# Optimization experiments

Measured on AMD Instinct MI355X. Metric: run time of the kernel, lower is better.

The kernel has to match this reference:

```python
import jax, jax.numpy as jnp
import numpy as np

N = 50000
E = 800000
IN_C = 128
HID = 8
OUT_C = 32
HEADS = (4, 4, 4)
NEG_SLOPE = 0.2


def gat_conv(x, src, dst, W, att_src, att_dst, bias, heads, out_c, concat):
    # x: [N, F_in]; W: [F_in, heads*out_c]; att_*: [heads, out_c]; bias: [heads*out_c] or [out_c]
    n = x.shape[0]
    h = (x @ W).reshape(n, heads, out_c)                      # [N, H, C]
    a_src = (h * att_src).sum(-1)                             # [N, H]
    a_dst = (h * att_dst).sum(-1)                             # [N, H]
    e = jax.nn.leaky_relu(a_src[src] + a_dst[dst], NEG_SLOPE)  # [E, H]
    # segment softmax over edges grouped by destination node
    m = jax.ops.segment_max(e, dst, num_segments=n)           # [N, H]
    m = jnp.where(jnp.isfinite(m), m, 0.0)
    p = jnp.exp(e - m[dst])                                   # [E, H]
    s = jax.ops.segment_sum(p, dst, num_segments=n)           # [N, H]
    alpha = p / (s[dst] + 1e-16)                              # [E, H]
    msg = h[src] * alpha[:, :, None]                          # [E, H, C]
    out = jax.ops.segment_sum(msg, dst, num_segments=n)       # [N, H, C]
    out = out.reshape(n, heads * out_c) if concat else out.mean(axis=1)
    return out + bias


def setup_inputs() -> dict:
    key = jax.random.key(0)
    ks = jax.random.split(key, 16)
    x = jax.random.normal(ks[0], (N, IN_C), dtype=jnp.float32)
    edge_index = jax.random.randint(ks[1], (2, E), 0, N, dtype=jnp.int64)
    c1 = HID                       # per-head out of conv1 (8)
    c2 = HID * HEADS[0]            # per-head out of conv2 (32)
    c3 = OUT_C                     # per-head out of conv3 (32)
    in2 = HID * HEADS[0]           # 32
    in3 = HID * HEADS[0] * HEADS[1]  # 128
    sc = 0.1
    return {
        "x": x,
        "edge_index": edge_index,
        "W1": jax.random.normal(ks[2], (IN_C, HEADS[0] * c1), dtype=jnp.float32) * sc,
        "as1": jax.random.normal(ks[3], (HEADS[0], c1), dtype=jnp.float32) * sc,
        "ad1": jax.random.normal(ks[4], (HEADS[0], c1), dtype=jnp.float32) * sc,
        "b1": jnp.zeros((HEADS[0] * c1,), dtype=jnp.float32),
        "W2": jax.random.normal(ks[5], (in2, HEADS[1] * c2), dtype=jnp.float32) * sc,
        "as2": jax.random.normal(ks[6], (HEADS[1], c2), dtype=jnp.float32) * sc,
        "ad2": jax.random.normal(ks[7], (HEADS[1], c2), dtype=jnp.float32) * sc,
        "b2": jnp.zeros((HEADS[1] * c2,), dtype=jnp.float32),
        "W3": jax.random.normal(ks[8], (in3, HEADS[2] * c3), dtype=jnp.float32) * sc,
        "as3": jax.random.normal(ks[9], (HEADS[2], c3), dtype=jnp.float32) * sc,
        "ad3": jax.random.normal(ks[10], (HEADS[2], c3), dtype=jnp.float32) * sc,
        "b3": jnp.zeros((c3,), dtype=jnp.float32),
    }


def reference(x, edge_index, W1, as1, ad1, b1, W2, as2, ad2, b2, W3, as3, ad3, b3):
    src, dst = edge_index[0], edge_index[1]
    h = gat_conv(x, src, dst, W1, as1, ad1, b1, HEADS[0], HID, True)
    h = jax.nn.elu(h)
    h = gat_conv(h, src, dst, W2, as2, ad2, b2, HEADS[1], HID * HEADS[0], True)
    h = jax.nn.elu(h)
    out = gat_conv(h, src, dst, W3, as3, ad3, b3, HEADS[2], OUT_C, False)
    return out
```

## Files before the change

kernel.cpp:

```cpp
#include <hip/hip_runtime.h>
#include <hip/hip_fp16.h>

#define NEG_SLOPE 0.2f

static inline int cdiv(long long a, long long b) { return (int)((a + b - 1) / b); }

typedef _Float16 f16x8 __attribute__((ext_vector_type(8)));
typedef float f32x4 __attribute__((ext_vector_type(4)));

union h4u {
    float2  f2;
    __half2 h2[2];
};
union h8u {
    f16x8   v;
    __half2 h2[4];
};

__device__ __forceinline__ void load_sd(const void* ei_raw, int is64, int e, int E_,
                                        int& s, int& d)
{
    if (is64) {
        const long long* p = (const long long*)ei_raw;
        s = (int)p[e];
        d = (int)p[E_ + e];
    } else {
        const int* p = (const int*)ei_raw;
        s = p[e];
        d = p[E_ + e];
    }
}

__global__ __launch_bounds__(256) void prep_kernel(
    const void* __restrict__ ei, int E_, int n, int* __restrict__ flag,
    int* __restrict__ deg,
    const float* __restrict__ W1, __half* __restrict__ Wt1,
    const float* __restrict__ W2, __half* __restrict__ Wt2,
    const float* __restrict__ W3, __half* __restrict__ Wt3)
{
    int idx = blockIdx.x * 256 + threadIdx.x;

    if (blockIdx.x == 0) {
        __shared__ int bad;
        if (threadIdx.x == 0) bad = 0;
        __syncthreads();
        const long long* e64 = (const long long*)ei;
        int cnt = E_ < 512 ? E_ : 512;
        bool ok = true;
        for (int i = threadIdx.x; i < cnt; i += 256) {
            long long v = e64[i];
            if (v < 0 || v >= n) ok = false;
        }
        if (!ok) atomicAdd(&bad, 1);
        __syncthreads();
        if (threadIdx.x == 0) *flag = (bad == 0) ? 1 : 0;
    }

    if (idx < n) deg[idx] = 0;

    if (idx < 128 * 32) {
        int k = idx / 32, c = idx % 32;
        Wt1[c * 128 + k] = __float2half(W1[idx]);
    }
    if (idx < 32 * 128) {
        int k = idx / 128, c = idx % 128;
        Wt2[c * 32 + k] = __float2half(W2[idx]);
    }
    if (idx < 128 * 128) {
        int k = idx / 128, c = idx % 128;
        Wt3[c * 128 + k] = __float2half(W3[idx]);
    }
}

__global__ __launch_bounds__(256) void hist_kernel(const void* __restrict__ ei_raw,
                                                   const int* __restrict__ flag,
                                                   int* __restrict__ deg,
                                                   unsigned short* __restrict__ s16,
                                                   unsigned short* __restrict__ d16,
                                                   unsigned short* __restrict__ r16,
                                                   int E_)
{
    int base = blockIdx.x * 1024 + threadIdx.x;
    int is64 = *flag;
    int sj[4], dj[4], rj[4];
    bool v[4];
#pragma unroll
    for (int j = 0; j < 4; j++) {
        int e = base + j * 256;
        v[j] = e < E_;
        if (v[j]) load_sd(ei_raw, is64, e, E_, sj[j], dj[j]);
    }
#pragma unroll
    for (int j = 0; j < 4; j++) {
        int e = base + j * 256;
        if (v[j]) {
            s16[e] = (unsigned short)sj[j];
            d16[e] = (unsigned short)dj[j];
        }
    }
#pragma unroll
    for (int j = 0; j < 4; j++) {
        if (v[j]) rj[j] = atomicAdd(deg + dj[j], 1);
    }
#pragma unroll
    for (int j = 0; j < 4; j++) {
        int e = base + j * 256;
        if (v[j]) r16[e] = (unsigned short)rj[j];
    }
}

__device__ __forceinline__ int wave_incl_scan(int v)
{
    int lane = threadIdx.x & 63;
#pragma unroll
    for (int off = 1; off < 64; off <<= 1) {
        int t = __shfl_up(v, off);
        if (lane >= off) v += t;
    }
    return v;
}

__global__ __launch_bounds__(1024) void scan_part_kernel(const int* __restrict__ deg,
                                                         int* __restrict__ start,
                                                         int* __restrict__ bsum, int n)
{
    __shared__ int wsum[16];
    int i = blockIdx.x * 1024 + threadIdx.x;
    int wid = threadIdx.x >> 6, lane = threadIdx.x & 63;
    int v = (i < n) ? deg[i] : 0;
    int incl = wave_incl_scan(v);
    if (lane == 63) wsum[wid] = incl;
    __syncthreads();
    if (wid == 0) {
        int w = (lane < 16) ? wsum[lane] : 0;
        w = wave_incl_scan(w);
        if (lane < 16) wsum[lane] = w;
    }
    __syncthreads();
    int excl = incl - v + (wid ? wsum[wid - 1] : 0);
    if (i < n) start[i] = excl;
    if (threadIdx.x == 1023) bsum[blockIdx.x] = wsum[15];
}

__global__ __launch_bounds__(1024) void scan_add_kernel(const int* __restrict__ deg,
                                                        const int* __restrict__ bsum,
                                                        int* __restrict__ start, int n)
{
    __shared__ int off_sh;
    if (threadIdx.x == 0) {
        int s = 0;
        for (int j = 0; j < blockIdx.x; j++) s += bsum[j];
        off_sh = s;
    }
    __syncthreads();
    int i = blockIdx.x * 1024 + threadIdx.x;
    if (i >= n) return;
    int v = start[i] + off_sh;
    start[i] = v;
    if (i == n - 1) start[n] = v + deg[i];
}

__global__ __launch_bounds__(256) void scatter_kernel(
    const unsigned short* __restrict__ s16, const unsigned short* __restrict__ d16,
    const unsigned short* __restrict__ r16, const int* __restrict__ start,
    unsigned short* __restrict__ sorted_src, int E_)
{
    int base = blockIdx.x * 1024 + threadIdx.x;
    int sj[4], dj[4], rj[4];
    bool v[4];
#pragma unroll
    for (int j = 0; j < 4; j++) {
        int e = base + j * 256;
        v[j] = e < E_;
        sj[j] = v[j] ? (int)s16[e] : 0;
        dj[j] = v[j] ? (int)d16[e] : 0;
        rj[j] = v[j] ? (int)r16[e] : 0;
    }
    int pj[4];
#pragma unroll
    for (int j = 0; j < 4; j++) {
        if (v[j]) pj[j] = start[dj[j]] + rj[j];
    }
#pragma unroll
    for (int j = 0; j < 4; j++) {
        if (v[j])
            __builtin_nontemporal_store((unsigned short)sj[j], sorted_src + pj[j]);
    }
}

template <int K, int NOUT, int A16>
__global__ __launch_bounds__(256) void gemm_mfma_kernel(
    const void* __restrict__ xin, const __half* __restrict__ Wt,
    const float* __restrict__ att_s, const float* __restrict__ att_d,
    __half* __restrict__ h, float* __restrict__ a_s, float* __restrict__ a_d, int n)
{
    constexpr int KC = 32;
    constexpr int NT = NOUT / 16;
    constexpr int XP = KC + 8;
    constexpr int HP = NOUT + 8;
    constexpr int C  = NOUT / 4;

    __shared__ _Float16 Xs[64 * XP];
    __shared__ _Float16 Ws[NOUT * XP];
    __shared__ _Float16 Hs[64 * HP];
    __shared__ float As[NOUT], Ad[NOUT];

    const int tid  = threadIdx.x;
    const int nb   = blockIdx.x * 64;
    const int wave = tid >> 6, lane = tid & 63;
    const int m16  = lane & 15, quad = lane >> 4;

    if (tid < NOUT) { As[tid] = att_s[tid]; Ad[tid] = att_d[tid]; }

    f32x4 acc[NT];
#pragma unroll
    for (int t = 0; t < NT; t++) acc[t] = (f32x4){0.f, 0.f, 0.f, 0.f};

    for (int kc = 0; kc < K; kc += KC) {
        {
            int node = tid >> 2, seg = tid & 3;
            int gn = nb + node;
            f16x8 v = {0, 0, 0, 0, 0, 0, 0, 0};
            if (gn < n) {
                if (A16) {
                    v = *(const f16x8*)((const __half*)xin + (size_t)gn * K + kc +
                                        seg * 8);
                } else {
                    const float4* p =
                        (const float4*)((const float*)xin + (size_t)gn * K + kc + seg * 8);
                    float4 a = p[0], b = p[1];
                    v = (f16x8){(_Float16)a.x, (_Float16)a.y, (_Float16)a.z,
                                (_Float16)a.w, (_Float16)b.x, (_Float16)b.y,
                                (_Float16)b.z, (_Float16)b.w};
                }
            }
            *(f16x8*)&Xs[node * XP + seg * 8] = v;
        }
        for (int u = tid; u < NOUT * 4; u += 256) {
            int col = u >> 2, seg = u & 3;
            *(f16x8*)&Ws[col * XP + seg * 8] =
                *(const f16x8*)(Wt + (size_t)col * K + kc + seg * 8);
        }
        __syncthreads();

        f16x8 a = *(const f16x8*)&Xs[(wave * 16 + m16) * XP + quad * 8];
#pragma unroll
        for (int t = 0; t < NT; t++) {
            f16x8 b = *(const f16x8*)&Ws[(t * 16 + m16) * XP + quad * 8];
            acc[t] = __builtin_amdgcn_mfma_f32_16x16x32_f16(a, b, acc[t], 0, 0, 0);
        }
        __syncthreads();
    }

#pragma unroll
    for (int t = 0; t < NT; t++) {
#pragma unroll
        for (int r = 0; r < 4; r++) {
            int row = wave * 16 + quad * 4 + r;
            Hs[row * HP + t * 16 + m16] = (_Float16)acc[t][r];
        }
    }
    __syncthreads();

    for (int u = tid; u < 64 * NOUT / 8; u += 256) {
        int row = u / (NOUT / 8), seg = u % (NOUT / 8);
        int gn = nb + row;
        if (gn < n)
            *(f16x8*)(h + (size_t)gn * NOUT + seg * 8) =
                *(const f16x8*)&Hs[row * HP + seg * 8];
    }

    {
        int node = tid >> 2, head = tid & 3;
        int gn = nb + node;
        const _Float16* hr = &Hs[node * HP + head * C];
        float s1 = 0.f, s2 = 0.f;
#pragma unroll 4
        for (int c = 0; c < C; c++) {
            float v = (float)hr[c];
            s1 += v * As[head * C + c];
            s2 += v * Ad[head * C + c];
        }
        if (gn < n) {
            a_s[gn * 4 + head] = s1;
            a_d[gn * 4 + head] = s2;
        }
    }
}

template <int MODE>
__global__ __launch_bounds__(256) void gat_agg128_kernel(
    const int* __restrict__ start, const unsigned short* __restrict__ ss,
    const __half* __restrict__ h, const float* __restrict__ a_s,
    const float* __restrict__ a_d, const float* __restrict__ bias,
    void* __restrict__ out, int n)
{
    int local = threadIdx.x >> 4;
    int q     = threadIdx.x & 15;
    int node  = blockIdx.x * 16 + local;
    bool active = node < n;
    int s0 = 0, s1 = 0;
    if (active) { s0 = start[node]; s1 = start[node + 1]; }
    int head = q >> 2;
    float adh = active ? a_d[node * 4 + head] : 0.f;
    const f16x8* __restrict__ h8 = (const f16x8*)h + q;

    float acc[8];
#pragma unroll
    for (int j = 0; j < 8; j++) acc[j] = 0.f;
    float sm = 0.f;

    int i = s0;
    for (; i + 8 <= s1; i += 8) {
        int   sj[8];
        float ej[8];
        h8u   rj[8];
#pragma unroll
        for (int j = 0; j < 8; j++) sj[j] = (int)ss[i + j];
#pragma unroll
        for (int j = 0; j < 8; j++) ej[j] = a_s[sj[j] * 4 + head];
#pragma unroll
        for (int j = 0; j < 8; j++) rj[j].v = h8[(size_t)sj[j] * 16];
#pragma unroll
        for (int j = 0; j < 8; j++) {
            float e = ej[j] + adh;
            e = e > 0.f ? e : NEG_SLOPE * e;
            float p = __expf(e);
            sm += p;
#pragma unroll
            for (int k = 0; k < 4; k++) {
                float2 f = __half22float2(rj[j].h2[k]);
                acc[2 * k]     += f.x * p;
                acc[2 * k + 1] += f.y * p;
            }
        }
    }
    for (; i < s1; i++) {
        int s = (int)ss[i];
        float e = a_s[s * 4 + head] + adh;
        e = e > 0.f ? e : NEG_SLOPE * e;
        float p = __expf(e);
        sm += p;
        h8u u; u.v = h8[(size_t)s * 16];
#pragma unroll
        for (int k = 0; k < 4; k++) {
            float2 f = __half22float2(u.h2[k]);
            acc[2 * k]     += f.x * p;
            acc[2 * k + 1] += f.y * p;
        }
    }

    float inv = 1.f / (sm + 1e-16f);
#pragma unroll
    for (int j = 0; j < 8; j++) acc[j] *= inv;

    if (MODE == 0) {
        if (active) {
            h8u u;
#pragma unroll
            for (int k = 0; k < 4; k++) {
                float vx = acc[2 * k]     + bias[q * 8 + 2 * k];
                float vy = acc[2 * k + 1] + bias[q * 8 + 2 * k + 1];
                vx = vx > 0.f ? vx : (__expf(vx) - 1.f);
                vy = vy > 0.f ? vy : (__expf(vy) - 1.f);
                u.h2[k] = __floats2half2_rn(vx, vy);
            }
            *(f16x8*)((__half*)out + (size_t)node * 128 + q * 8) = u.v;
        }
    } else {
        __shared__ float sh[16][132];
#pragma unroll
        for (int j = 0; j < 8; j++) sh[local][q * 8 + j] = acc[j];
        __syncthreads();
        if (q < 4 && active) {
            float r[8];
#pragma unroll
            for (int j = 0; j < 8; j++) {
                int c = q * 8 + j;
                r[j] = 0.25f * (sh[local][c] + sh[local][32 + c] + sh[local][64 + c] +
                                sh[local][96 + c]) + bias[c];
            }
            float4* o4 = (float4*)((float*)out + (size_t)node * 32 + q * 8);
            o4[0] = make_float4(r[0], r[1], r[2], r[3]);
            o4[1] = make_float4(r[4], r[5], r[6], r[7]);
        }
    }
}

__global__ __launch_bounds__(256) void gat_agg32_kernel(
    const int* __restrict__ start, const unsigned short* __restrict__ ss,
    const __half* __restrict__ h, const float* __restrict__ a_s,
    const float* __restrict__ a_d, const float* __restrict__ bias,
    __half* __restrict__ out, int n)
{
    int local = threadIdx.x >> 2;
    int q     = threadIdx.x & 3;
    int node  = blockIdx.x * 64 + local;
    bool active = node < n;
    int s0 = 0, s1 = 0;
    if (active) { s0 = start[node]; s1 = start[node + 1]; }
    float adh = active ? a_d[node * 4 + q] : 0.f;
    const f16x8* __restrict__ h8 = (const f16x8*)h + q;

    float acc[8];
#pragma unroll
    for (int j = 0; j < 8; j++) acc[j] = 0.f;
    float sm = 0.f;

    int i = s0;
    for (; i + 8 <= s1; i += 8) {
        int   sj[8];
        float ej[8];
        h8u   rj[8];
#pragma unroll
        for (int j = 0; j < 8; j++) sj[j] = (int)ss[i + j];
#pragma unroll
        for (int j = 0; j < 8; j++) ej[j] = a_s[sj[j] * 4 + q];
#pragma unroll
        for (int j = 0; j < 8; j++) rj[j].v = h8[(size_t)sj[j] * 4];
#pragma unroll
        for (int j = 0; j < 8; j++) {
            float e = ej[j] + adh;
            e = e > 0.f ? e : NEG_SLOPE * e;
            float p = __expf(e);
            sm += p;
#pragma unroll
            for (int k = 0; k < 4; k++) {
                float2 f = __half22float2(rj[j].h2[k]);
                acc[2 * k]     += f.x * p;
                acc[2 * k + 1] += f.y * p;
            }
        }
    }
    for (; i < s1; i++) {
        int s = (int)ss[i];
        float e = a_s[s * 4 + q] + adh;
        e = e > 0.f ? e : NEG_SLOPE * e;
        float p = __expf(e);
        sm += p;
        h8u u; u.v = h8[(size_t)s * 4];
#pragma unroll
        for (int k = 0; k < 4; k++) {
            float2 f = __half22float2(u.h2[k]);
            acc[2 * k]     += f.x * p;
            acc[2 * k + 1] += f.y * p;
        }
    }

    if (active) {
        float inv = 1.f / (sm + 1e-16f);
        h8u u;
#pragma unroll
        for (int k = 0; k < 4; k++) {
            float vx = acc[2 * k] * inv     + bias[q * 8 + 2 * k];
            float vy = acc[2 * k + 1] * inv + bias[q * 8 + 2 * k + 1];
            vx = vx > 0.f ? vx : (__expf(vx) - 1.f);
            vy = vy > 0.f ? vy : (__expf(vy) - 1.f);
            u.h2[k] = __floats2half2_rn(vx, vy);
        }
        *(f16x8*)(out + (size_t)node * 32 + q * 8) = u.v;
    }
}


extern "C" void kernel_launch(void* const* d_in, const int* in_sizes, int n_in,
                              void* d_out, int out_size, void* d_ws, size_t ws_size,
                              hipStream_t stream)
{
    const float* x   = (const float*)d_in[0];
    const void*  ei  = d_in[1];
    const float* W1  = (const float*)d_in[2];
    const float* as1 = (const float*)d_in[3];
    const float* ad1 = (const float*)d_in[4];
    const float* b1  = (const float*)d_in[5];
    const float* W2  = (const float*)d_in[6];
    const float* as2 = (const float*)d_in[7];
    const float* ad2 = (const float*)d_in[8];
    const float* b2  = (const float*)d_in[9];
    const float* W3  = (const float*)d_in[10];
    const float* as3 = (const float*)d_in[11];
    const float* ad3 = (const float*)d_in[12];
    const float* b3  = (const float*)d_in[13];
    float* out = (float*)d_out;

    const int N_ = in_sizes[0] / 128;
    const int E_ = in_sizes[1] / 2;

    char* ws = (char*)d_ws;
    size_t off = 0;
    auto alloc = [&](size_t nbytes) -> void* {
        void* p = ws + off;
        off += (nbytes + 255) & ~(size_t)255;
        return p;
    };
    __half* h          = (__half*)alloc((size_t)N_ * 128 * 2);
    __half* x2h        = (__half*)alloc((size_t)N_ * 32 * 2);
    __half* x3h        = (__half*)alloc((size_t)N_ * 128 * 2);
    __half* Wt1        = (__half*)alloc(128 * 32 * 2);
    __half* Wt2        = (__half*)alloc(32 * 128 * 2);
    __half* Wt3        = (__half*)alloc(128 * 128 * 2);
    float* asrc        = (float*)alloc((size_t)N_ * 4 * 4);
    float* adst        = (float*)alloc((size_t)N_ * 4 * 4);
    int*   deg         = (int*)alloc((size_t)N_ * 4);
    int*   start       = (int*)alloc((size_t)(N_ + 1) * 4);
    unsigned short* sorted_src = (unsigned short*)alloc((size_t)E_ * 2);
    unsigned short* s16        = (unsigned short*)alloc((size_t)E_ * 2);
    unsigned short* d16        = (unsigned short*)alloc((size_t)E_ * 2);
    unsigned short* r16        = (unsigned short*)alloc((size_t)E_ * 2);
    int*   bsum        = (int*)alloc(4096);
    int*   flag        = (int*)alloc(256);

    const int gN16 = cdiv(N_, 16);
    const int gN64 = cdiv(N_, 64);
    const int nSB  = cdiv(N_, 1024);
    int prepWork = N_ > 128 * 128 ? N_ : 128 * 128;

    prep_kernel<<<cdiv(prepWork, 256), 256, 0, stream>>>(ei, E_, N_, flag, deg,
                                                         W1, Wt1, W2, Wt2, W3, Wt3);
    hist_kernel<<<cdiv(E_, 1024), 256, 0, stream>>>(ei, flag, deg, s16, d16, r16, E_);
    scan_part_kernel<<<nSB, 1024, 0, stream>>>(deg, start, bsum, N_);
    scan_add_kernel<<<nSB, 1024, 0, stream>>>(deg, bsum, start, N_);
    scatter_kernel<<<cdiv(E_, 1024), 256, 0, stream>>>(s16, d16, r16, start,
                                                       sorted_src, E_);

    gemm_mfma_kernel<128, 32, 0><<<gN64, 256, 0, stream>>>(x, Wt1, as1, ad1, h,
                                                           asrc, adst, N_);
    gat_agg32_kernel<<<gN64, 256, 0, stream>>>(start, sorted_src, h, asrc, adst, b1,
                                               x2h, N_);

    gemm_mfma_kernel<32, 128, 1><<<gN64, 256, 0, stream>>>(x2h, Wt2, as2, ad2, h,
                                                           asrc, adst, N_);
    gat_agg128_kernel<0><<<gN16, 256, 0, stream>>>(start, sorted_src, h, asrc, adst, b2,
                                                   x3h, N_);

    gemm_mfma_kernel<128, 128, 1><<<gN64, 256, 0, stream>>>(x3h, Wt3, as3, ad3, h,
                                                            asrc, adst, N_);
    gat_agg128_kernel<1><<<gN16, 256, 0, stream>>>(start, sorted_src, h, asrc, adst, b3,
                                                   out, N_);
}
```

Before: 282.5 us.

## Fuse GAT aggregations with following GEMMs and merge layer-1 GEMM into histogram

New measurement: 286.3 us. No clear change (+1.4%).

```diff
diff --git a/kernel.cpp b/kernel.cpp
--- a/kernel.cpp
+++ b/kernel.cpp
@@ -8,10 +8,6 @@
 typedef _Float16 f16x8 __attribute__((ext_vector_type(8)));
 typedef float f32x4 __attribute__((ext_vector_type(4)));
 
-union h4u {
-    float2  f2;
-    __half2 h2[2];
-};
 union h8u {
     f16x8   v;
     __half2 h2[4];
@@ -72,40 +68,125 @@
     }
 }
 
-__global__ __launch_bounds__(256) void hist_kernel(const void* __restrict__ ei_raw,
-                                                   const int* __restrict__ flag,
-                                                   int* __restrict__ deg,
-                                                   unsigned short* __restrict__ s16,
-                                                   unsigned short* __restrict__ d16,
-                                                   unsigned short* __restrict__ r16,
-                                                   int E_)
-{
-    int base = blockIdx.x * 1024 + threadIdx.x;
-    int is64 = *flag;
-    int sj[4], dj[4], rj[4];
-    bool v[4];
-#pragma unroll
-    for (int j = 0; j < 4; j++) {
-        int e = base + j * 256;
-        v[j] = e < E_;
-        if (v[j]) load_sd(ei_raw, is64, e, E_, sj[j], dj[j]);
-    }
-#pragma unroll
-    for (int j = 0; j < 4; j++) {
-        int e = base + j * 256;
-        if (v[j]) {
-            s16[e] = (unsigned short)sj[j];
-            d16[e] = (unsigned short)dj[j];
-        }
-    }
-#pragma unroll
-    for (int j = 0; j < 4; j++) {
-        if (v[j]) rj[j] = atomicAdd(deg + dj[j], 1);
-    }
-#pragma unroll
-    for (int j = 0; j < 4; j++) {
-        int e = base + j * 256;
-        if (v[j]) r16[e] = (unsigned short)rj[j];
+__global__ __launch_bounds__(256) void gemm1_hist_kernel(
+    const float* __restrict__ x, const __half* __restrict__ Wt1,
+    const float* __restrict__ att_s, const float* __restrict__ att_d,
+    __half* __restrict__ h, float* __restrict__ a_s, float* __restrict__ a_d,
+    int n, int gemmBlocks,
+    const void* __restrict__ ei, const int* __restrict__ flag,
+    int* __restrict__ deg, unsigned short* __restrict__ s16,
+    unsigned short* __restrict__ d16, unsigned short* __restrict__ r16, int E_)
+{
+    constexpr int KC = 32, NT = 2, XP = 40, HP = 40, C = 8;
+    __shared__ _Float16 Xs[64 * XP];
+    __shared__ _Float16 Ws[32 * XP];
+    __shared__ _Float16 Hs[64 * HP];
+    __shared__ float As[32], Ad[32];
+
+    const int tid = threadIdx.x;
+
+    if (blockIdx.x >= gemmBlocks) {
+        int base = (blockIdx.x - gemmBlocks) * 1024 + tid;
+        int is64 = *flag;
+        int sj[4], dj[4], rj[4];
+        bool v[4];
+#pragma unroll
+        for (int j = 0; j < 4; j++) {
+            int e = base + j * 256;
+            v[j] = e < E_;
+            if (v[j]) load_sd(ei, is64, e, E_, sj[j], dj[j]);
+        }
+#pragma unroll
+        for (int j = 0; j < 4; j++) {
+            int e = base + j * 256;
+            if (v[j]) {
+                s16[e] = (unsigned short)sj[j];
+                d16[e] = (unsigned short)dj[j];
+            }
+        }
+#pragma unroll
+        for (int j = 0; j < 4; j++) {
+            if (v[j]) rj[j] = atomicAdd(deg + dj[j], 1);
+        }
+#pragma unroll
+        for (int j = 0; j < 4; j++) {
+            int e = base + j * 256;
+            if (v[j]) r16[e] = (unsigned short)rj[j];
+        }
+        return;
+    }
+
+    const int nb   = blockIdx.x * 64;
+    const int wave = tid >> 6, lane = tid & 63;
+    const int m16  = lane & 15, quad = lane >> 4;
+
+    if (tid < 32) { As[tid] = att_s[tid]; Ad[tid] = att_d[tid]; }
+
+    f32x4 acc[NT];
+#pragma unroll
+    for (int t = 0; t < NT; t++) acc[t] = (f32x4){0.f, 0.f, 0.f, 0.f};
+
+    for (int kc = 0; kc < 128; kc += KC) {
+        {
+            int node = tid >> 2, seg = tid & 3;
+            int gn = nb + node;
+            f16x8 v = {0, 0, 0, 0, 0, 0, 0, 0};
+            if (gn < n) {
+                const float4* p = (const float4*)(x + (size_t)gn * 128 + kc + seg * 8);
+                float4 a = p[0], b = p[1];
+                v = (f16x8){(_Float16)a.x, (_Float16)a.y, (_Float16)a.z, (_Float16)a.w,
+                            (_Float16)b.x, (_Float16)b.y, (_Float16)b.z, (_Float16)b.w};
+            }
+            *(f16x8*)&Xs[node * XP + seg * 8] = v;
+        }
+        if (tid < 32 * 4) {
+            int col = tid >> 2, seg = tid & 3;
+            *(f16x8*)&Ws[col * XP + seg * 8] =
+                *(const f16x8*)(Wt1 + (size_t)col * 128 + kc + seg * 8);
+        }
+        __syncthreads();
+
+        f16x8 a = *(const f16x8*)&Xs[(wave * 16 + m16) * XP + quad * 8];
+#pragma unroll
+        for (int t = 0; t < NT; t++) {
+            f16x8 b = *(const f16x8*)&Ws[(t * 16 + m16) * XP + quad * 8];
+            acc[t] = __builtin_amdgcn_mfma_f32_16x16x32_f16(a, b, acc[t], 0, 0, 0);
+        }
+        __syncthreads();
+    }
+
+#pragma unroll
+    for (int t = 0; t < NT; t++) {
+#pragma unroll
+        for (int r = 0; r < 4; r++) {
+            int row = wave * 16 + quad * 4 + r;
+            Hs[row * HP + t * 16 + m16] = (_Float16)acc[t][r];
+        }
+    }
+    __syncthreads();
+
+    if (tid < 64 * 4) {
+        int row = tid >> 2, seg = tid & 3;
+        int gn = nb + row;
+        if (gn < n)
+            *(f16x8*)(h + (size_t)gn * 32 + seg * 8) = *(const f16x8*)&Hs[row * HP + seg * 8];
+    }
+
+    {
+        int node = tid >> 2, head = tid & 3;
+        int gn = nb + node;
+        const _Float16* hr = &Hs[node * HP + head * C];
+        float s1 = 0.f, s2 = 0.f;
+#pragma unroll
+        for (int c = 0; c < C; c++) {
+            float v = (float)hr[c];
+            s1 += v * As[head * C + c];
+            s2 += v * Ad[head * C + c];
+        }
+        if (gn < n) {
+            a_s[gn * 4 + head] = s1;
+            a_d[gn * 4 + head] = s2;
+        }
     }
 }
 
@@ -188,62 +269,269 @@
     }
 }
 
-template <int K, int NOUT, int A16>
-__global__ __launch_bounds__(256) void gemm_mfma_kernel(
-    const void* __restrict__ xin, const __half* __restrict__ Wt,
-    const float* __restrict__ att_s, const float* __restrict__ att_d,
-    __half* __restrict__ h, float* __restrict__ a_s, float* __restrict__ a_d, int n)
-{
-    constexpr int KC = 32;
-    constexpr int NT = NOUT / 16;
-    constexpr int XP = KC + 8;
-    constexpr int HP = NOUT + 8;
-    constexpr int C  = NOUT / 4;
-
+__global__ __launch_bounds__(256) void agg32_gemm2_kernel(
+    const int* __restrict__ start, const unsigned short* __restrict__ ss,
+    const __half* __restrict__ h_in, const float* __restrict__ a_s,
+    const float* __restrict__ a_d, const float* __restrict__ b1,
+    const __half* __restrict__ Wt2, const float* __restrict__ as2,
+    const float* __restrict__ ad2, __half* __restrict__ h_out,
+    float* __restrict__ a_s2, float* __restrict__ a_d2, int n)
+{
+    constexpr int XP = 40, HP = 136, NT = 8;
     __shared__ _Float16 Xs[64 * XP];
-    __shared__ _Float16 Ws[NOUT * XP];
+    __shared__ _Float16 Ws[128 * XP];
     __shared__ _Float16 Hs[64 * HP];
-    __shared__ float As[NOUT], Ad[NOUT];
-
-    const int tid  = threadIdx.x;
-    const int nb   = blockIdx.x * 64;
+    __shared__ float As[128], Ad[128];
+
+    const int tid = threadIdx.x;
+    const int nb  = blockIdx.x * 64;
+
+    if (tid < 128) { As[tid] = as2[tid]; Ad[tid] = ad2[tid]; }
+
+    {
+        int local = tid >> 2;
+        int q     = tid & 3;
+        int node  = nb + local;
+        bool active = node < n;
+        int s0 = 0, s1 = 0;
+        if (active) { s0 = start[node]; s1 = start[node + 1]; }
+        float adh = active ? a_d[node * 4 + q] : 0.f;
+        const f16x8* __restrict__ h8 = (const f16x8*)h_in + q;
+
+        float acc[8];
+#pragma unroll
+        for (int j = 0; j < 8; j++) acc[j] = 0.f;
+        float sm = 0.f;
+
+        int i = s0;
+        for (; i + 8 <= s1; i += 8) {
+            int   sj[8];
+            float ej[8];
+            h8u   rj[8];
+#pragma unroll
+            for (int j = 0; j < 8; j++) sj[j] = (int)ss[i + j];
+#pragma unroll
+            for (int j = 0; j < 8; j++) ej[j] = a_s[sj[j] * 4 + q];
+#pragma unroll
+            for (int j = 0; j < 8; j++) rj[j].v = h8[(size_t)sj[j] * 4];
+#pragma unroll
+            for (int j = 0; j < 8; j++) {
+                float e = ej[j] + adh;
+                e = e > 0.f ? e : NEG_SLOPE * e;
+                float p = __expf(e);
+                sm += p;
+#pragma unroll
+                for (int k = 0; k < 4; k++) {
+                    float2 f = __half22float2(rj[j].h2[k]);
+                    acc[2 * k]     += f.x * p;
+                    acc[2 * k + 1] += f.y * p;
+                }
+            }
+        }
+        for (; i < s1; i++) {
+            int s = (int)ss[i];
+            float e = a_s[s * 4 + q] + adh;
+            e = e > 0.f ? e : NEG_SLOPE * e;
+            float p = __expf(e);
+            sm += p;
+            h8u u; u.v = h8[(size_t)s * 4];
+#pragma unroll
+            for (int k = 0; k < 4; k++) {
+                float2 f = __half22float2(u.h2[k]);
+                acc[2 * k]     += f.x * p;
+                acc[2 * k + 1] += f.y * p;
+            }
+        }
+
+        h8u o;
+        if (active) {
+            float inv = 1.f / (sm + 1e-16f);
+#pragma unroll
+            for (int k = 0; k < 4; k++) {
+                float vx = acc[2 * k] * inv     + b1[q * 8 + 2 * k];
+                float vy = acc[2 * k + 1] * inv + b1[q * 8 + 2 * k + 1];
+                vx = vx > 0.f ? vx : (__expf(vx) - 1.f);
+                vy = vy > 0.f ? vy : (__expf(vy) - 1.f);
+                o.h2[k] = __floats2half2_rn(vx, vy);
+            }
+        } else {
+            o.v = (f16x8){0, 0, 0, 0, 0, 0, 0, 0};
+        }
+        *(f16x8*)&Xs[local * XP + q * 8] = o.v;
+    }
+
+    if (tid < 128 * 4 / 2) {
+    }
+    for (int u = tid; u < 128 * 4; u += 256) {
+        int col = u >> 2, seg = u & 3;
+        *(f16x8*)&Ws[col * XP + seg * 8] =
+            *(const f16x8*)(Wt2 + (size_t)col * 32 + seg * 8);
+    }
+    __syncthreads();
+
     const int wave = tid >> 6, lane = tid & 63;
     const int m16  = lane & 15, quad = lane >> 4;
 
-    if (tid < NOUT) { As[tid] = att_s[tid]; Ad[tid] = att_d[tid]; }
-
     f32x4 acc[NT];
 #pragma unroll
     for (int t = 0; t < NT; t++) acc[t] = (f32x4){0.f, 0.f, 0.f, 0.f};
 
-    for (int kc = 0; kc < K; kc += KC) {
-        {
-            int node = tid >> 2, seg = tid & 3;
-            int gn = nb + node;
-            f16x8 v = {0, 0, 0, 0, 0, 0, 0, 0};
-            if (gn < n) {
-                if (A16) {
-                    v = *(const f16x8*)((const __half*)xin + (size_t)gn * K + kc +
-                                        seg * 8);
-                } else {
-                    const float4* p =
-                        (const float4*)((const float*)xin + (size_t)gn * K + kc + seg * 8);
-                    float4 a = p[0], b = p[1];
-                    v = (f16x8){(_Float16)a.x, (_Float16)a.y, (_Float16)a.z,
-                                (_Float16)a.w, (_Float16)b.x, (_Float16)b.y,
-                                (_Float16)b.z, (_Float16)b.w};
+    f16x8 a = *(const f16x8*)&Xs[(wave * 16 + m16) * XP + quad * 8];
+#pragma unroll
+    for (int t = 0; t < NT; t++) {
+        f16x8 b = *(const f16x8*)&Ws[(t * 16 + m16) * XP + quad * 8];
+        acc[t] = __builtin_amdgcn_mfma_f32_16x16x32_f16(a, b, acc[t], 0, 0, 0);
+    }
+    __syncthreads();
+
+#pragma unroll
+    for (int t = 0; t < NT; t++) {
+#pragma unroll
+        for (int r = 0; r < 4; r++) {
+            int row = wave * 16 + quad * 4 + r;
+            Hs[row * HP + t * 16 + m16] = (_Float16)acc[t][r];
+        }
+    }
+    __syncthreads();
+
+    for (int u = tid; u < 64 * 16; u += 256) {
+        int row = u >> 4, seg = u & 15;
+        int gn = nb + row;
+        if (gn < n)
+            *(f16x8*)(h_out + (size_t)gn * 128 + seg * 8) =
+                *(const f16x8*)&Hs[row * HP + seg * 8];
+    }
+
+    {
+        int node = tid >> 2, head = tid & 3;
+        int gn = nb + node;
+        const _Float16* hr = &Hs[node * HP + head * 32];
+        float s1 = 0.f, s2 = 0.f;
+#pragma unroll 4
+        for (int c = 0; c < 32; c++) {
+            float v = (float)hr[c];
+            s1 += v * As[head * 32 + c];
+            s2 += v * Ad[head * 32 + c];
+        }
+        if (gn < n) {
+            a_s2[gn * 4 + head] = s1;
+            a_d2[gn * 4 + head] = s2;
+        }
+    }
+}
+
+__global__ __launch_bounds__(256) void agg128_gemm3_kernel(
+    const int* __restrict__ start, const unsigned short* __restrict__ ss,
+    const __half* __restrict__ h_in, const float* __restrict__ a_s,
+    const float* __restrict__ a_d, const float* __restrict__ b2,
+    const __half* __restrict__ Wt3, const float* __restrict__ as3,
+    const float* __restrict__ ad3, __half* __restrict__ h_out,
+    float* __restrict__ a_s3, float* __restrict__ a_d3, int n)
+{
+    constexpr int XAP = 136, XP = 40, HP = 136, NT = 8;
+    __shared__ _Float16 Xs[64 * XAP];
+    __shared__ _Float16 Ws[128 * XP];
+    __shared__ _Float16 Hs[64 * HP];
+    __shared__ float As[128], Ad[128];
+
+    const int tid = threadIdx.x;
+    const int nb  = blockIdx.x * 64;
+
+    if (tid < 128) { As[tid] = as3[tid]; Ad[tid] = ad3[tid]; }
+
+    {
+        int grp = tid >> 4;
+        int q   = tid & 15;
+        int head = q >> 2;
+        const f16x8* __restrict__ h8 = (const f16x8*)h_in + q;
+
+        for (int it = 0; it < 4; it++) {
+            int local = it * 16 + grp;
+            int node  = nb + local;
+            bool active = node < n;
+            int s0 = 0, s1 = 0;
+            if (active) { s0 = start[node]; s1 = start[node + 1]; }
+            float adh = active ? a_d[node * 4 + head] : 0.f;
+
+            float acc[8];
+#pragma unroll
+            for (int j = 0; j < 8; j++) acc[j] = 0.f;
+            float sm = 0.f;
+
+            int i = s0;
+            for (; i + 8 <= s1; i += 8) {
+                int   sj[8];
+                float ej[8];
+                h8u   rj[8];
+#pragma unroll
+                for (int j = 0; j < 8; j++) sj[j] = (int)ss[i + j];
+#pragma unroll
+                for (int j = 0; j < 8; j++) ej[j] = a_s[sj[j] * 4 + head];
+#pragma unroll
+                for (int j = 0; j < 8; j++) rj[j].v = h8[(size_t)sj[j] * 16];
+#pragma unroll
+                for (int j = 0; j < 8; j++) {
+                    float e = ej[j] + adh;
+                    e = e > 0.f ? e : NEG_SLOPE * e;
+                    float p = __expf(e);
+                    sm += p;
+#pragma unroll
+                    for (int k = 0; k < 4; k++) {
+                        float2 f = __half22float2(rj[j].h2[k]);
+                        acc[2 * k]     += f.x * p;
+                        acc[2 * k + 1] += f.y * p;
+                    }
                 }
             }
-            *(f16x8*)&Xs[node * XP + seg * 8] = v;
-        }
-        for (int u = tid; u < NOUT * 4; u += 256) {
+            for (; i < s1; i++) {
+                int s = (int)ss[i];
+                float e = a_s[s * 4 + head] + adh;
+                e = e > 0.f ? e : NEG_SLOPE * e;
+                float p = __expf(e);
+                sm += p;
+                h8u u; u.v = h8[(size_t)s * 16];
+#pragma unroll
+                for (int k = 0; k < 4; k++) {
+                    float2 f = __half22float2(u.h2[k]);
+                    acc[2 * k]     += f.x * p;
+                    acc[2 * k + 1] += f.y * p;
+                }
+            }
+
+            h8u o;
+            if (active) {
+                float inv = 1.f / (sm + 1e-16f);
+#pragma unroll
+                for (int k = 0; k < 4; k++) {
+                    float vx = acc[2 * k] * inv     + b2[q * 8 + 2 * k];
+                    float vy = acc[2 * k + 1] * inv + b2[q * 8 + 2 * k + 1];
+                    vx = vx > 0.f ? vx : (__expf(vx) - 1.f);
+                    vy = vy > 0.f ? vy : (__expf(vy) - 1.f);
+                    o.h2[k] = __floats2half2_rn(vx, vy);
+                }
+            } else {
+                o.v = (f16x8){0, 0, 0, 0, 0, 0, 0, 0};
+            }
+            *(f16x8*)&Xs[local * XAP + q * 8] = o.v;
+        }
+    }
+
+    const int wave = tid >> 6, lane = tid & 63;
+    const int m16  = lane & 15, quad = lane >> 4;
+
+    f32x4 acc[NT];
+#pragma unroll
+    for (int t = 0; t < NT; t++) acc[t] = (f32x4){0.f, 0.f, 0.f, 0.f};
+
+    for (int kc = 0; kc < 128; kc += 32) {
+        for (int u = tid; u < 128 * 4; u += 256) {
             int col = u >> 2, seg = u & 3;
             *(f16x8*)&Ws[col * XP + seg * 8] =
-                *(const f16x8*)(Wt + (size_t)col * K + kc + seg * 8);
+                *(const f16x8*)(Wt3 + (size_t)col * 128 + kc + seg * 8);
         }
         __syncthreads();
 
-        f16x8 a = *(const f16x8*)&Xs[(wave * 16 + m16) * XP + quad * 8];
+        f16x8 a = *(const f16x8*)&Xs[(wave * 16 + m16) * XAP + kc + quad * 8];
 #pragma unroll
         for (int t = 0; t < NT; t++) {
             f16x8 b = *(const f16x8*)&Ws[(t * 16 + m16) * XP + quad * 8];
@@ -262,38 +550,37 @@
     }
     __syncthreads();
 
-    for (int u = tid; u < 64 * NOUT / 8; u += 256) {
-        int row = u / (NOUT / 8), seg = u % (NOUT / 8);
+    for (int u = tid; u < 64 * 16; u += 256) {
+        int row = u >> 4, seg = u & 15;
         int gn = nb + row;
         if (gn < n)
-            *(f16x8*)(h + (size_t)gn * NOUT + seg * 8) =
+            *(f16x8*)(h_out + (size_t)gn * 128 + seg * 8) =
                 *(const f16x8*)&Hs[row * HP + seg * 8];
     }
 
     {
         int node = tid >> 2, head = tid & 3;
         int gn = nb + node;
-        const _Float16* hr = &Hs[node * HP + head * C];
+        const _Float16* hr = &Hs[node * HP + head * 32];
         float s1 = 0.f, s2 = 0.f;
 #pragma unroll 4
-        for (int c = 0; c < C; c++) {
+        for (int c = 0; c < 32; c++) {
             float v = (float)hr[c];
-            s1 += v * As[head * C + c];
-            s2 += v * Ad[head * C + c];
+            s1 += v * As[head * 32 + c];
+            s2 += v * Ad[head * 32 + c];
         }
         if (gn < n) {
-            a_s[gn * 4 + head] = s1;
-            a_d[gn * 4 + head] = s2;
-        }
-    }
-}
-
-template <int MODE>
-__global__ __launch_bounds__(256) void gat_agg128_kernel(
+            a_s3[gn * 4 + head] = s1;
+            a_d3[gn * 4 + head] = s2;
+        }
+    }
+}
+
+__global__ __launch_bounds__(256) void gat_agg_final_kernel(
     const int* __restrict__ start, const unsigned short* __restrict__ ss,
     const __half* __restrict__ h, const float* __restrict__ a_s,
     const float* __restrict__ a_d, const float* __restrict__ bias,
-    void* __restrict__ out, int n)
+    float* __restrict__ out, int n)
 {
     int local = threadIdx.x >> 4;
     int q     = threadIdx.x & 15;
@@ -354,111 +641,21 @@
 #pragma unroll
     for (int j = 0; j < 8; j++) acc[j] *= inv;
 
-    if (MODE == 0) {
-        if (active) {
-            h8u u;
-#pragma unroll
-            for (int k = 0; k < 4; k++) {
-                float vx = acc[2 * k]     + bias[q * 8 + 2 * k];
-                float vy = acc[2 * k + 1] + bias[q * 8 + 2 * k + 1];
-                vx = vx > 0.f ? vx : (__expf(vx) - 1.f);
-                vy = vy > 0.f ? vy : (__expf(vy) - 1.f);
-                u.h2[k] = __floats2half2_rn(vx, vy);
-            }
-            *(f16x8*)((__half*)out + (size_t)node * 128 + q * 8) = u.v;
-        }
-    } else {
-        __shared__ float sh[16][132];
-#pragma unroll
-        for (int j = 0; j < 8; j++) sh[local][q * 8 + j] = acc[j];
-        __syncthreads();
-        if (q < 4 && active) {
-            float r[8];
-#pragma unroll
-            for (int j = 0; j < 8; j++) {
-                int c = q * 8 + j;
-                r[j] = 0.25f * (sh[local][c] + sh[local][32 + c] + sh[local][64 + c] +
-                                sh[local][96 + c]) + bias[c];
-            }
-            float4* o4 = (float4*)((float*)out + (size_t)node * 32 + q * 8);
-            o4[0] = make_float4(r[0], r[1], r[2], r[3]);
-            o4[1] = make_float4(r[4], r[5], r[6], r[7]);
-        }
-    }
-}
-
-__global__ __launch_bounds__(256) void gat_agg32_kernel(
-    const int* __restrict__ start, const unsigned short* __restrict__ ss,
-    const __half* __restrict__ h, const float* __restrict__ a_s,
-    const float* __restrict__ a_d, const float* __restrict__ bias,
-    __half* __restrict__ out, int n)
-{
-    int local = threadIdx.x >> 2;
-    int q     = threadIdx.x & 3;
-    int node  = blockIdx.x * 64 + local;
-    bool active = node < n;
-    int s0 = 0, s1 = 0;
-    if (active) { s0 = start[node]; s1 = start[node + 1]; }
-    float adh = active ? a_d[node * 4 + q] : 0.f;
-    const f16x8* __restrict__ h8 = (const f16x8*)h + q;
-
-    float acc[8];
-#pragma unroll
-    for (int j = 0; j < 8; j++) acc[j] = 0.f;
-    float sm = 0.f;
-
-    int i = s0;
-    for (; i + 8 <= s1; i += 8) {
-        int   sj[8];
-        float ej[8];
-        h8u   rj[8];
-#pragma unroll
-        for (int j = 0; j < 8; j++) sj[j] = (int)ss[i + j];
-#pragma unroll
-        for (int j = 0; j < 8; j++) ej[j] = a_s[sj[j] * 4 + q];
-#pragma unroll
-        for (int j = 0; j < 8; j++) rj[j].v = h8[(size_t)sj[j] * 4];
+    __shared__ float sh[16][132];
+#pragma unroll
+    for (int j = 0; j < 8; j++) sh[local][q * 8 + j] = acc[j];
+    __syncthreads();
+    if (q < 4 && active) {
+        float r[8];
 #pragma unroll
         for (int j = 0; j < 8; j++) {
-            float e = ej[j] + adh;
-            e = e > 0.f ? e : NEG_SLOPE * e;
-            float p = __expf(e);
-            sm += p;
-#pragma unroll
-            for (int k = 0; k < 4; k++) {
-                float2 f = __half22float2(rj[j].h2[k]);
-                acc[2 * k]     += f.x * p;
-                acc[2 * k + 1] += f.y * p;
-            }
-        }
-    }
-    for (; i < s1; i++) {
-        int s = (int)ss[i];
-        float e = a_s[s * 4 + q] + adh;
-        e = e > 0.f ? e : NEG_SLOPE * e;
-        float p = __expf(e);
-        sm += p;
-        h8u u; u.v = h8[(size_t)s * 4];
-#pragma unroll
-        for (int k = 0; k < 4; k++) {
-            float2 f = __half22float2(u.h2[k]);
-            acc[2 * k]     += f.x * p;
-            acc[2 * k + 1] += f.y * p;
-        }
-    }
-
-    if (active) {
-        float inv = 1.f / (sm + 1e-16f);
-        h8u u;
-#pragma unroll
-        for (int k = 0; k < 4; k++) {
-            float vx = acc[2 * k] * inv     + bias[q * 8 + 2 * k];
-            float vy = acc[2 * k + 1] * inv + bias[q * 8 + 2 * k + 1];
-            vx = vx > 0.f ? vx : (__expf(vx) - 1.f);
-            vy = vy > 0.f ? vy : (__expf(vy) - 1.f);
-            u.h2[k] = __floats2half2_rn(vx, vy);
-        }
-        *(f16x8*)(out + (size_t)node * 32 + q * 8) = u.v;
+            int c = q * 8 + j;
+            r[j] = 0.25f * (sh[local][c] + sh[local][32 + c] + sh[local][64 + c] +
+                            sh[local][96 + c]) + bias[c];
+        }
+        float4* o4 = (float4*)(out + (size_t)node * 32 + q * 8);
+        o4[0] = make_float4(r[0], r[1], r[2], r[3]);
+        o4[1] = make_float4(r[4], r[5], r[6], r[7]);
     }
 }
 
@@ -493,14 +690,15 @@
         off += (nbytes + 255) & ~(size_t)255;
         return p;
     };
-    __half* h          = (__half*)alloc((size_t)N_ * 128 * 2);
-    __half* x2h        = (__half*)alloc((size_t)N_ * 32 * 2);
-    __half* x3h        = (__half*)alloc((size_t)N_ * 128 * 2);
+    __half* hA         = (__half*)alloc((size_t)N_ * 128 * 2);
+    __half* hB         = (__half*)alloc((size_t)N_ * 128 * 2);
     __half* Wt1        = (__half*)alloc(128 * 32 * 2);
     __half* Wt2        = (__half*)alloc(32 * 128 * 2);
     __half* Wt3        = (__half*)alloc(128 * 128 * 2);
-    float* asrc        = (float*)alloc((size_t)N_ * 4 * 4);
-    float* adst        = (float*)alloc((size_t)N_ * 4 * 4);
+    float* asA         = (float*)alloc((size_t)N_ * 4 * 4);
+    float* adA         = (float*)alloc((size_t)N_ * 4 * 4);
+    float* asB         = (float*)alloc((size_t)N_ * 4 * 4);
+    float* adB         = (float*)alloc((size_t)N_ * 4 * 4);
     int*   deg         = (int*)alloc((size_t)N_ * 4);
     int*   start       = (int*)alloc((size_t)(N_ + 1) * 4);
     unsigned short* sorted_src = (unsigned short*)alloc((size_t)E_ * 2);
@@ -512,29 +710,26 @@
 
     const int gN16 = cdiv(N_, 16);
     const int gN64 = cdiv(N_, 64);
+    const int gHist = cdiv(E_, 1024);
     const int nSB  = cdiv(N_, 1024);
     int prepWork = N_ > 128 * 128 ? N_ : 128 * 128;
 
     prep_kernel<<<cdiv(prepWork, 256), 256, 0, stream>>>(ei, E_, N_, flag, deg,
                                                          W1, Wt1, W2, Wt2, W3, Wt3);
-    hist_kernel<<<cdiv(E_, 1024), 256, 0, stream>>>(ei, flag, deg, s16, d16, r16, E_);
+    gemm1_hist_kernel<<<gN64 + gHist, 256, 0, stream>>>(
+        x, Wt1, as1, ad1, hA, asA, adA, N_, gN64,
+        ei, flag, deg, s16, d16, r16, E_);
     scan_part_kernel<<<nSB, 1024, 0, stream>>>(deg, start, bsum, N_);
     scan_add_kernel<<<nSB, 1024, 0, stream>>>(deg, bsum, start, N_);
     scatter_kernel<<<cdiv(E_, 1024), 256, 0, stream>>>(s16, d16, r16, start,
                                                        sorted_src, E_);
 
-    gemm_mfma_kernel<128, 32, 0><<<gN64, 256, 0, stream>>>(x, Wt1, as1, ad1, h,
-                                                           asrc, adst, N_);
-    gat_agg32_kernel<<<gN64, 256, 0, stream>>>(start, sorted_src, h, asrc, adst, b1,
-                                               x2h, N_);
-
-    gemm_mfma_kernel<32, 128, 1><<<gN64, 256, 0, stream>>>(x2h, Wt2, as2, ad2, h,
-                                                           asrc, adst, N_);
-    gat_agg128_kernel<0><<<gN16, 256, 0, stream>>>(start, sorted_src, h, asrc, adst, b2,
-                                                   x3h, N_);
-
-    gemm_mfma_kernel<128, 128, 1><<<gN64, 256, 0, stream>>>(x3h, Wt3, as3, ad3, h,
-                                                            asrc, adst, N_);
-    gat_agg128_kernel<1><<<gN16, 256, 0, stream>>>(start, sorted_src, h, asrc, adst, b3,
+    agg32_gemm2_kernel<<<gN64, 256, 0, stream>>>(start, sorted_src, hA, asA, adA, b1,
+                                                 Wt2, as2, ad2, hB, asB, adB, N_);
+
+    agg128_gemm3_kernel<<<gN64, 256, 0, stream>>>(start, sorted_src, hB, asB, adB, b2,
+                                                  Wt3, as3, ad3, hA, asA, adA, N_);
+
+    gat_agg_final_kernel<<<gN16, 256, 0, stream>>>(start, sorted_src, hA, asA, adA, b3,
                                                    out, N_);
 }
```
